# Kernel tuning notes

Measured on AMD Instinct MI355X. Metric: run time of the kernel, lower is better.

Reference implementation:

```python
import jax, jax.numpy as jnp
import numpy as np

# Static config matching init_kwargs
K0, K1 = 3, 3          # kernel_size
S0, S1 = 1, 1          # stride
P0, P1 = 1, 1          # padding
L_IN, L_OUT = 4, 8     # capsule lengths
ITERS = 3              # routing iterations


def setup_inputs() -> dict:
    key = jax.random.key(0)
    kx, kw = jax.random.split(key)
    x = jax.random.normal(kx, (4, 32, 56, 56), dtype=jnp.float32)
    # weight: (out_channels//out_length, in_channels//in_length * kH*kW, in_length, out_length)
    weight = jax.random.normal(kw, (8, 8 * K0 * K1, L_IN, L_OUT), dtype=jnp.float32)
    return {"x": x, "weight": weight}


def squash(t, axis=-1):
    norm = jnp.linalg.norm(t, axis=axis, keepdims=True)
    return (norm / (1.0 + norm ** 2)) * t


def reference(x, weight):
    N, C, H, W = x.shape
    H_out = 1 + (H + 2 * P0 - K0) // S0
    W_out = 1 + (W + 2 * P1 - K1) // S1
    G_in = C // L_IN
    G_out = weight.shape[0]
    kk = K0 * K1

    xp = jnp.pad(x, ((0, 0), (0, 0), (P0, P0), (P1, P1)))
    # im2col: stack kernel offsets (k0-major, k1-minor, matching torch unfold order)
    patches = jnp.stack(
        [xp[:, :, i:i + S0 * H_out:S0, j:j + S1 * W_out:S1]
         for i in range(K0) for j in range(K1)], axis=0)          # (kk, N, C, Ho, Wo)
    patches = patches.reshape(kk, N, G_in, L_IN, H_out, W_out)
    # -> (N, P, G_in, kk, L_in) with P = Ho*Wo
    xwin = jnp.transpose(patches, (1, 4, 5, 2, 0, 3)).reshape(
        N, H_out * W_out, G_in, kk, L_IN)

    w = weight.reshape(G_out, G_in, kk, L_IN, L_OUT)
    # priors: (G_out, N, P, G_in, kk, L_out)
    priors = jnp.einsum('npgkl,cgklm->cnpgkm', xwin, w)

    # dynamic routing
    logits = jnp.zeros_like(priors)
    v = None
    for r in range(ITERS):
        probs = jax.nn.softmax(logits, axis=-2)                    # over kk dim
        s = jnp.sum(probs * priors, axis=(-3, -2), keepdims=True)  # sum over G_in, kk
        v = squash(s, axis=-1)                                     # (G_out,N,P,1,1,L_out)
        if r != ITERS - 1:
            logits = logits + jnp.sum(priors * v, axis=-1, keepdims=True)

    out = v[:, :, :, 0, 0, :]                  # (G_out, N, P, L_out)
    out = jnp.transpose(out, (1, 0, 3, 2))     # (N, G_out, L_out, P)
    return out.reshape(N, G_out * L_OUT, H_out, W_out)
```

## Files before the change

kernel.cpp:

```cpp
#include <hip/hip_runtime.h>

#define NB   4
#define CIN  32
#define HH   56
#define WW   56
#define GIN  8
#define GOUT 8
#define LIN  4
#define LOUT 8
#define KK   9
#define HW   (HH * WW)
#define PIXTOT (NB * HW)
#define PPB  32
#define WSLICE (GIN * KK * LIN * LOUT)
#define WS_G 292
#define HP   58
#define WP   58

typedef float v2f __attribute__((ext_vector_type(2)));
typedef float v4f __attribute__((ext_vector_type(4)));

static __device__ __forceinline__ v2f fma2(v2f a, v2f b, v2f c) {
    return __builtin_elementwise_fma(a, b, c);
}

__global__ __launch_bounds__(256) void transpose_x_kernel(
    const float* __restrict__ x, float* __restrict__ xt)
{
    __shared__ float tile[CIN * 57];
    const int b = blockIdx.x;
    const int n = b / HP;
    const int hp = b - n * HP;
    const int h = hp - 1;
    const int tid = threadIdx.x;
    const bool rowok = (unsigned)h < (unsigned)HH;

    if (rowok) {
        for (int i = tid; i < CIN * WW; i += 256) {
            const int ch = i / WW;
            const int w  = i - ch * WW;
            tile[ch * 57 + w] = x[((n * CIN + ch) * HH + h) * WW + w];
        }
    }
    __syncthreads();
    float* dst = xt + ((size_t)(n * HP + hp) * WP) * CIN;
    for (int i = tid; i < WP * CIN; i += 256) {
        const int wp = i >> 5;
        const int ch = i & 31;
        const bool ok = rowok && (wp >= 1) && (wp <= WW);
        dst[i] = ok ? tile[ch * 57 + (wp - 1)] : 0.0f;
    }
}

__global__ __launch_bounds__(256) void caps_routing_kernel(
    const float* __restrict__ xt, const float* __restrict__ wt,
    float* __restrict__ out)
{
    __shared__ __align__(16) float ws[GIN * WS_G];

    const int tid = threadIdx.x;
    const int c = blockIdx.y;

    const int g  = tid & 7;
    const int pl = tid >> 3;
    const int pix = blockIdx.x * PPB + pl;
    const int n = pix / HW;
    const int p = pix - n * HW;
    const int h = p / WW;
    const int w = p - h * WW;

    v4f xv4[KK];
    const float* base = xt + ((size_t)((n * HP + h) * WP + w)) * CIN + g * 4;
    #pragma unroll
    for (int ki = 0; ki < 3; ++ki)
        #pragma unroll
        for (int kj = 0; kj < 3; ++kj)
            xv4[ki * 3 + kj] =
                *reinterpret_cast<const v4f*>(base + (ki * WP + kj) * CIN);

    {
        const int gg = tid >> 5;
        const int r0 = tid & 31;
        const float* src = wt + c * WSLICE + gg * 288;
        float* dst = ws + gg * WS_G;
        #pragma unroll
        for (int j = 0; j < 9; ++j)
            dst[r0 + j * 32] = src[r0 + j * 32];
    }
    __syncthreads();

    v2f pr2[KK][4];
    v2f ks2[4] = {v2f{0.f,0.f}, v2f{0.f,0.f}, v2f{0.f,0.f}, v2f{0.f,0.f}};

    const float* wg = &ws[g * WS_G];
    #pragma unroll
    for (int k = 0; k < KK; ++k) {
        v2f a0 = {0.f,0.f}, a1 = {0.f,0.f}, a2 = {0.f,0.f}, a3 = {0.f,0.f};
        #pragma unroll
        for (int l = 0; l < LIN; ++l) {
            const float xs = xv4[k][l];
            const v2f xs2 = {xs, xs};
            const v4f w01 = *reinterpret_cast<const v4f*>(wg + k * 32 + l * 8);
            const v4f w23 = *reinterpret_cast<const v4f*>(wg + k * 32 + l * 8 + 4);
            a0 = fma2(xs2, __builtin_shufflevector(w01, w01, 0, 1), a0);
            a1 = fma2(xs2, __builtin_shufflevector(w01, w01, 2, 3), a1);
            a2 = fma2(xs2, __builtin_shufflevector(w23, w23, 0, 1), a2);
            a3 = fma2(xs2, __builtin_shufflevector(w23, w23, 2, 3), a3);
        }
        pr2[k][0] = a0; pr2[k][1] = a1; pr2[k][2] = a2; pr2[k][3] = a3;
        ks2[0] += a0; ks2[1] += a1; ks2[2] += a2; ks2[3] += a3;
    }

    float logits[KK];
    #pragma unroll
    for (int k = 0; k < KK; ++k) logits[k] = 0.0f;

    v2f v2[4];
    #pragma unroll
    for (int it = 0; it < 3; ++it) {
        v2f s2[4];
        if (it == 0) {
            #pragma unroll
            for (int j = 0; j < 4; ++j) s2[j] = ks2[j] * (1.0f / 9.0f);
        } else {
            float e[KK];
            float sum = 0.0f;
            #pragma unroll
            for (int k = 0; k < KK; ++k) { e[k] = __expf(logits[k]); sum += e[k]; }
            const float inv = 1.0f / sum;
            #pragma unroll
            for (int j = 0; j < 4; ++j) s2[j] = v2f{0.f, 0.f};
            #pragma unroll
            for (int k = 0; k < KK; ++k) {
                const v2f ek = {e[k], e[k]};
                #pragma unroll
                for (int j = 0; j < 4; ++j) s2[j] = fma2(ek, pr2[k][j], s2[j]);
            }
            const v2f inv2 = {inv, inv};
            #pragma unroll
            for (int j = 0; j < 4; ++j) s2[j] *= inv2;
        }

        #pragma unroll
        for (int off = 1; off < 8; off <<= 1) {
            #pragma unroll
            for (int j = 0; j < 4; ++j) {
                s2[j].x += __shfl_xor(s2[j].x, off, 64);
                s2[j].y += __shfl_xor(s2[j].y, off, 64);
            }
        }

        v2f t = s2[0] * s2[0];
        t = fma2(s2[1], s2[1], t);
        t = fma2(s2[2], s2[2], t);
        t = fma2(s2[3], s2[3], t);
        const float n2 = t.x + t.y;
        const float f = sqrtf(n2) / (1.0f + n2);
        const v2f f2 = {f, f};
        #pragma unroll
        for (int j = 0; j < 4; ++j) v2[j] = f2 * s2[j];

        if (it != 2) {
            #pragma unroll
            for (int k = 0; k < KK; ++k) {
                v2f d2 = pr2[k][0] * v2[0];
                d2 = fma2(pr2[k][1], v2[1], d2);
                d2 = fma2(pr2[k][2], v2[2], d2);
                d2 = fma2(pr2[k][3], v2[3], d2);
                logits[k] += d2.x + d2.y;
            }
        }
    }

    const float vs[8] = { v2[0].x, v2[0].y, v2[1].x, v2[1].y,
                          v2[2].x, v2[2].y, v2[3].x, v2[3].y };
    float outv = vs[0];
    #pragma unroll
    for (int m = 1; m < LOUT; ++m) if (g == m) outv = vs[m];
    out[(n * GOUT * LOUT + c * LOUT + g) * HW + p] = outv;
}

extern "C" void kernel_launch(void* const* d_in, const int* in_sizes, int n_in,
                              void* d_out, int out_size, void* d_ws, size_t ws_size,
                              hipStream_t stream) {
    const float* x  = (const float*)d_in[0];
    const float* wt = (const float*)d_in[1];
    float* out = (float*)d_out;
    float* xt = (float*)d_ws;

    transpose_x_kernel<<<dim3(NB * HP), dim3(256), 0, stream>>>(x, xt);
    dim3 grid(PIXTOT / PPB, GOUT);
    caps_routing_kernel<<<grid, dim3(256), 0, stream>>>(xt, wt, out);
}
```

Measured before the change: 34.29 us.

## Process two pixels per thread and use DPP for the capsule-group reduction

Each thread now handles two pixels, so every weight vector read from LDS is reused for both pixels and the block covers 64 pixels, halving the grid and the per-block weight staging. The cross-lane sum over the 8 input groups is done with DPP row operations instead of __shfl_xor, which avoids the LDS-based permute path. Launch bounds request two blocks per CU. Register pressure roughly doubles for priors and logits, which could cut occupancy or cause spills.

```diff
diff --git a/kernel.cpp b/kernel.cpp
--- a/kernel.cpp
+++ b/kernel.cpp
@@ -4,15 +4,15 @@
 #define CIN  32
 #define HH   56
 #define WW   56
-#define GIN  8
 #define GOUT 8
 #define LIN  4
 #define LOUT 8
 #define KK   9
 #define HW   (HH * WW)
 #define PIXTOT (NB * HW)
-#define PPB  32
-#define WSLICE (GIN * KK * LIN * LOUT)
+#define PXT  2
+#define PPB  64
+#define WSLICE 2304
 #define WS_G 292
 #define HP   58
 #define WP   58
@@ -23,6 +23,10 @@
 static __device__ __forceinline__ v2f fma2(v2f a, v2f b, v2f c) {
     return __builtin_elementwise_fma(a, b, c);
 }
+
+#define DPP_XADD(x, CTRL) \
+    (x) += __int_as_float(__builtin_amdgcn_update_dpp( \
+        0, __float_as_int(x), (CTRL), 0xF, 0xF, true))
 
 __global__ __launch_bounds__(256) void transpose_x_kernel(
     const float* __restrict__ x, float* __restrict__ xt)
@@ -52,31 +56,37 @@
     }
 }
 
-__global__ __launch_bounds__(256) void caps_routing_kernel(
+__global__ __launch_bounds__(256, 2) void caps_routing_kernel(
     const float* __restrict__ xt, const float* __restrict__ wt,
     float* __restrict__ out)
 {
-    __shared__ __align__(16) float ws[GIN * WS_G];
+    __shared__ __align__(16) float ws[8 * WS_G];
 
     const int tid = threadIdx.x;
     const int c = blockIdx.y;
 
-    const int g  = tid & 7;
-    const int pl = tid >> 3;
-    const int pix = blockIdx.x * PPB + pl;
-    const int n = pix / HW;
-    const int p = pix - n * HW;
-    const int h = p / WW;
-    const int w = p - h * WW;
-
-    v4f xv4[KK];
-    const float* base = xt + ((size_t)((n * HP + h) * WP + w)) * CIN + g * 4;
-    #pragma unroll
-    for (int ki = 0; ki < 3; ++ki)
-        #pragma unroll
-        for (int kj = 0; kj < 3; ++kj)
-            xv4[ki * 3 + kj] =
-                *reinterpret_cast<const v4f*>(base + (ki * WP + kj) * CIN);
+    const int g    = tid & 7;
+    const int slot = tid >> 3;
+    int pixq[PXT];
+    pixq[0] = blockIdx.x * PPB + slot;
+    pixq[1] = pixq[0] + 32;
+
+    v4f xv4[PXT][KK];
+    #pragma unroll
+    for (int q = 0; q < PXT; ++q) {
+        const int pix = pixq[q];
+        const int n = pix / HW;
+        const int p = pix - n * HW;
+        const int h = p / WW;
+        const int w = p - h * WW;
+        const float* base = xt + ((size_t)((n * HP + h) * WP + w)) * CIN + g * 4;
+        #pragma unroll
+        for (int ki = 0; ki < 3; ++ki)
+            #pragma unroll
+            for (int kj = 0; kj < 3; ++kj)
+                xv4[q][ki * 3 + kj] =
+                    *reinterpret_cast<const v4f*>(base + (ki * WP + kj) * CIN);
+    }
 
     {
         const int gg = tid >> 5;
@@ -89,95 +99,137 @@
     }
     __syncthreads();
 
-    v2f pr2[KK][4];
-    v2f ks2[4] = {v2f{0.f,0.f}, v2f{0.f,0.f}, v2f{0.f,0.f}, v2f{0.f,0.f}};
+    v2f pr2[PXT][KK][4];
+    v2f ks2[PXT][4];
+    #pragma unroll
+    for (int q = 0; q < PXT; ++q)
+        #pragma unroll
+        for (int j = 0; j < 4; ++j) ks2[q][j] = v2f{0.f, 0.f};
 
     const float* wg = &ws[g * WS_G];
     #pragma unroll
     for (int k = 0; k < KK; ++k) {
-        v2f a0 = {0.f,0.f}, a1 = {0.f,0.f}, a2 = {0.f,0.f}, a3 = {0.f,0.f};
+        v2f a[PXT][4];
+        #pragma unroll
+        for (int q = 0; q < PXT; ++q)
+            #pragma unroll
+            for (int j = 0; j < 4; ++j) a[q][j] = v2f{0.f, 0.f};
         #pragma unroll
         for (int l = 0; l < LIN; ++l) {
-            const float xs = xv4[k][l];
-            const v2f xs2 = {xs, xs};
             const v4f w01 = *reinterpret_cast<const v4f*>(wg + k * 32 + l * 8);
             const v4f w23 = *reinterpret_cast<const v4f*>(wg + k * 32 + l * 8 + 4);
-            a0 = fma2(xs2, __builtin_shufflevector(w01, w01, 0, 1), a0);
-            a1 = fma2(xs2, __builtin_shufflevector(w01, w01, 2, 3), a1);
-            a2 = fma2(xs2, __builtin_shufflevector(w23, w23, 0, 1), a2);
-            a3 = fma2(xs2, __builtin_shufflevector(w23, w23, 2, 3), a3);
-        }
-        pr2[k][0] = a0; pr2[k][1] = a1; pr2[k][2] = a2; pr2[k][3] = a3;
-        ks2[0] += a0; ks2[1] += a1; ks2[2] += a2; ks2[3] += a3;
-    }
-
-    float logits[KK];
-    #pragma unroll
-    for (int k = 0; k < KK; ++k) logits[k] = 0.0f;
-
-    v2f v2[4];
+            const v2f wp0 = __builtin_shufflevector(w01, w01, 0, 1);
+            const v2f wp1 = __builtin_shufflevector(w01, w01, 2, 3);
+            const v2f wp2 = __builtin_shufflevector(w23, w23, 0, 1);
+            const v2f wp3 = __builtin_shufflevector(w23, w23, 2, 3);
+            #pragma unroll
+            for (int q = 0; q < PXT; ++q) {
+                const float xs = xv4[q][k][l];
+                const v2f xs2 = {xs, xs};
+                a[q][0] = fma2(xs2, wp0, a[q][0]);
+                a[q][1] = fma2(xs2, wp1, a[q][1]);
+                a[q][2] = fma2(xs2, wp2, a[q][2]);
+                a[q][3] = fma2(xs2, wp3, a[q][3]);
+            }
+        }
+        #pragma unroll
+        for (int q = 0; q < PXT; ++q)
+            #pragma unroll
+            for (int j = 0; j < 4; ++j) {
+                pr2[q][k][j] = a[q][j];
+                ks2[q][j] += a[q][j];
+            }
+    }
+
+    float logits[PXT][KK];
+    #pragma unroll
+    for (int q = 0; q < PXT; ++q)
+        #pragma unroll
+        for (int k = 0; k < KK; ++k) logits[q][k] = 0.0f;
+
+    v2f vv[PXT][4];
     #pragma unroll
     for (int it = 0; it < 3; ++it) {
-        v2f s2[4];
+        v2f s2[PXT][4];
         if (it == 0) {
             #pragma unroll
-            for (int j = 0; j < 4; ++j) s2[j] = ks2[j] * (1.0f / 9.0f);
+            for (int q = 0; q < PXT; ++q)
+                #pragma unroll
+                for (int j = 0; j < 4; ++j) s2[q][j] = ks2[q][j] * (1.0f / 9.0f);
         } else {
-            float e[KK];
-            float sum = 0.0f;
-            #pragma unroll
-            for (int k = 0; k < KK; ++k) { e[k] = __expf(logits[k]); sum += e[k]; }
-            const float inv = 1.0f / sum;
-            #pragma unroll
-            for (int j = 0; j < 4; ++j) s2[j] = v2f{0.f, 0.f};
-            #pragma unroll
-            for (int k = 0; k < KK; ++k) {
-                const v2f ek = {e[k], e[k]};
-                #pragma unroll
-                for (int j = 0; j < 4; ++j) s2[j] = fma2(ek, pr2[k][j], s2[j]);
+            #pragma unroll
+            for (int q = 0; q < PXT; ++q) {
+                float e[KK];
+                float sum = 0.0f;
+                #pragma unroll
+                for (int k = 0; k < KK; ++k) { e[k] = __expf(logits[q][k]); sum += e[k]; }
+                const float inv = 1.0f / sum;
+                #pragma unroll
+                for (int j = 0; j < 4; ++j) s2[q][j] = v2f{0.f, 0.f};
+                #pragma unroll
+                for (int k = 0; k < KK; ++k) {
+                    const v2f ek = {e[k], e[k]};
+                    #pragma unroll
+                    for (int j = 0; j < 4; ++j) s2[q][j] = fma2(ek, pr2[q][k][j], s2[q][j]);
+                }
+                const v2f inv2 = {inv, inv};
+                #pragma unroll
+                for (int j = 0; j < 4; ++j) s2[q][j] *= inv2;
             }
-            const v2f inv2 = {inv, inv};
-            #pragma unroll
-            for (int j = 0; j < 4; ++j) s2[j] *= inv2;
-        }
-
-        #pragma unroll
-        for (int off = 1; off < 8; off <<= 1) {
-            #pragma unroll
-            for (int j = 0; j < 4; ++j) {
-                s2[j].x += __shfl_xor(s2[j].x, off, 64);
-                s2[j].y += __shfl_xor(s2[j].y, off, 64);
-            }
-        }
-
-        v2f t = s2[0] * s2[0];
-        t = fma2(s2[1], s2[1], t);
-        t = fma2(s2[2], s2[2], t);
-        t = fma2(s2[3], s2[3], t);
-        const float n2 = t.x + t.y;
-        const float f = sqrtf(n2) / (1.0f + n2);
-        const v2f f2 = {f, f};
-        #pragma unroll
-        for (int j = 0; j < 4; ++j) v2[j] = f2 * s2[j];
+        }
+
+        #pragma unroll
+        for (int q = 0; q < PXT; ++q)
+            #pragma unroll
+            for (int j = 0; j < 4; ++j) { DPP_XADD(s2[q][j].x, 0xB1); DPP_XADD(s2[q][j].y, 0xB1); }
+        #pragma unroll
+        for (int q = 0; q < PXT; ++q)
+            #pragma unroll
+            for (int j = 0; j < 4; ++j) { DPP_XADD(s2[q][j].x, 0x4E); DPP_XADD(s2[q][j].y, 0x4E); }
+        #pragma unroll
+        for (int q = 0; q < PXT; ++q)
+            #pragma unroll
+            for (int j = 0; j < 4; ++j) { DPP_XADD(s2[q][j].x, 0x141); DPP_XADD(s2[q][j].y, 0x141); }
+
+        #pragma unroll
+        for (int q = 0; q < PXT; ++q) {
+            v2f t = s2[q][0] * s2[q][0];
+            t = fma2(s2[q][1], s2[q][1], t);
+            t = fma2(s2[q][2], s2[q][2], t);
+            t = fma2(s2[q][3], s2[q][3], t);
+            const float n2 = t.x + t.y;
+            const float f = sqrtf(n2) / (1.0f + n2);
+            const v2f f2 = {f, f};
+            #pragma unroll
+            for (int j = 0; j < 4; ++j) vv[q][j] = f2 * s2[q][j];
+        }
 
         if (it != 2) {
             #pragma unroll
-            for (int k = 0; k < KK; ++k) {
-                v2f d2 = pr2[k][0] * v2[0];
-                d2 = fma2(pr2[k][1], v2[1], d2);
-                d2 = fma2(pr2[k][2], v2[2], d2);
-                d2 = fma2(pr2[k][3], v2[3], d2);
-                logits[k] += d2.x + d2.y;
-            }
-        }
-    }
-
-    const float vs[8] = { v2[0].x, v2[0].y, v2[1].x, v2[1].y,
-                          v2[2].x, v2[2].y, v2[3].x, v2[3].y };
-    float outv = vs[0];
-    #pragma unroll
-    for (int m = 1; m < LOUT; ++m) if (g == m) outv = vs[m];
-    out[(n * GOUT * LOUT + c * LOUT + g) * HW + p] = outv;
+            for (int q = 0; q < PXT; ++q)
+                #pragma unroll
+                for (int k = 0; k < KK; ++k) {
+                    v2f d2 = pr2[q][k][0] * vv[q][0];
+                    d2 = fma2(pr2[q][k][1], vv[q][1], d2);
+                    d2 = fma2(pr2[q][k][2], vv[q][2], d2);
+                    d2 = fma2(pr2[q][k][3], vv[q][3], d2);
+                    logits[q][k] += d2.x + d2.y;
+                }
+        }
+    }
+
+    #pragma unroll
+    for (int q = 0; q < PXT; ++q) {
+        const float vs[8] = { vv[q][0].x, vv[q][0].y, vv[q][1].x, vv[q][1].y,
+                              vv[q][2].x, vv[q][2].y, vv[q][3].x, vv[q][3].y };
+        float outv = vs[0];
+        #pragma unroll
+        for (int m = 1; m < LOUT; ++m) if (g == m) outv = vs[m];
+        const int pix = pixq[q];
+        const int n = pix / HW;
+        const int p = pix - n * HW;
+        out[(n * GOUT * LOUT + c * LOUT + g) * HW + p] = outv;
+    }
 }
 
 extern "C" void kernel_launch(void* const* d_in, const int* in_sizes, int n_in,
```

After: 33.53 us. 1.02x faster.
